# Optimization experiments

Hardware: AMD Instinct MI355X
Metric: run time of the kernel (lower is better)

The kernel has to match this reference:

```python
import jax, jax.numpy as jnp
import numpy as np

T, H, I, E, K = 4096, 2048, 1408, 8, 2


def setup_inputs() -> dict:
    key = jax.random.key(0)
    k1, k2, k3, k4, k5, k6 = jax.random.split(key, 6)
    hidden_states = jax.random.normal(k1, (T, H), dtype=jnp.float32)
    top_k_index = jax.random.randint(k2, (T, K), 0, E, dtype=jnp.int32)
    top_k_weights = jax.random.uniform(k3, (T, K), dtype=jnp.float32)
    # nn.Linear stores weight as [out_features, in_features]
    s_h = 1.0 / np.sqrt(H)
    s_i = 1.0 / np.sqrt(I)
    gate_w = jax.random.uniform(k4, (E, I, H), dtype=jnp.float32, minval=-s_h, maxval=s_h)
    up_w = jax.random.uniform(k5, (E, I, H), dtype=jnp.float32, minval=-s_h, maxval=s_h)
    down_w = jax.random.uniform(k6, (E, H, I), dtype=jnp.float32, minval=-s_i, maxval=s_i)
    return {
        "hidden_states": hidden_states,
        "top_k_index": top_k_index,
        "top_k_weights": top_k_weights,
        "gate_w": gate_w,
        "up_w": up_w,
        "down_w": down_w,
    }


def reference(hidden_states, top_k_index, top_k_weights, gate_w, up_w, down_w):
    # combine[t, e] = sum_k top_k_weights[t, k] * 1[top_k_index[t, k] == e]
    num_experts = gate_w.shape[0]
    one_hot = jax.nn.one_hot(top_k_index, num_experts, dtype=hidden_states.dtype)  # [T, K, E]
    combine = jnp.einsum("tk,tke->te", top_k_weights, one_hot)  # [T, E]

    # dense-equivalent of per-expert gather -> SwiGLU MLP -> scatter-add
    gate = jnp.einsum("th,eih->tei", hidden_states, gate_w)  # [T, E, I]
    up = jnp.einsum("th,eih->tei", hidden_states, up_w)      # [T, E, I]
    inter = jax.nn.silu(gate) * up                               # [T, E, I]
    out = jnp.einsum("te,tei,ehi->th", combine, inter, down_w)  # [T, H]
    return out
```

## Files before the change

kernel.cpp:

```cpp
#include <hip/hip_runtime.h>
#include <cstdint>
#include <cstddef>

#define T_TOK 4096
#define HD 2048
#define ID 1408
#define NE 8
#define NA (T_TOK * 2)
#define MAXR 9216
#define MAXT 80
#define EIH ((size_t)NE * ID * HD)
#define N4 ((int)(EIH / 4))
#define NCGU 2048
#define NCASTD 1024
#define NTILE_M (MAXR / 128)

typedef __bf16 bf16x8 __attribute__((ext_vector_type(8)));
typedef float f32x4 __attribute__((ext_vector_type(4)));

__device__ __forceinline__ unsigned short f2bf(float f) {
  union { float f; unsigned int u; } c; c.f = f;
  unsigned int u = c.u;
  u += 0x7fffu + ((u >> 16) & 1u);
  return (unsigned short)(u >> 16);
}

__device__ __forceinline__ void gl_lds16(const unsigned short* g, unsigned short* l) {
  __builtin_amdgcn_global_load_lds(
      (const __attribute__((address_space(1))) unsigned int*)g,
      (__attribute__((address_space(3))) unsigned int*)l, 16, 0, 0);
}

__device__ __forceinline__ int swz_off(int R, int fq) {
  int q = ((R & 1) << 2) | fq;
  int p = q ^ ((R >> 1) & 7);
  return (R >> 1) * 64 + p * 8;
}

__global__ void moe_count(const int* __restrict__ idx, int* __restrict__ cnt) {
  int a = blockIdx.x * 256 + threadIdx.x;
  if (a < NA) atomicAdd(&cnt[idx[a]], 1);
}

__global__ void moe_scan(const int* __restrict__ cnt, int* __restrict__ seg,
                         int* __restrict__ work_e, int* __restrict__ work_r,
                         int* __restrict__ ntiles) {
  if (blockIdx.x == 0 && threadIdx.x == 0) {
    int off = 0, nt = 0;
    for (int e = 0; e < NE; ++e) {
      seg[e] = off;
      int c = cnt[e];
      int tiles = (c + 127) >> 7;
      for (int tb = 0; tb < tiles; ++tb) {
        work_e[nt] = e;
        work_r[nt] = off + tb * 128;
        ++nt;
      }
      off += tiles << 7;
    }
    *ntiles = nt;
  }
}

__global__ void moe_fill(const int* __restrict__ idx, const float* __restrict__ wts,
                         const int* __restrict__ seg, int* __restrict__ cnt2,
                         int* __restrict__ row_token, float* __restrict__ row_weight,
                         int* __restrict__ slot_of) {
  int a = blockIdx.x * 256 + threadIdx.x;
  if (a < NA) {
    int e = idx[a];
    int pos = atomicAdd(&cnt2[e], 1);
    int slot = seg[e] + pos;
    row_token[slot] = a >> 1;
    row_weight[slot] = wts[a];
    slot_of[a] = slot;
  }
}

__global__ void mega_gather_castgu(
    const float* __restrict__ hidden, const int* __restrict__ slot_of,
    unsigned short* __restrict__ Xg,
    const float* __restrict__ gate_w, const float* __restrict__ up_w,
    unsigned short* __restrict__ gate_bf, unsigned short* __restrict__ ub_out) {
  const int bx = blockIdx.x;
  if (bx < NA) {
    const int slot = slot_of[bx];
    const int t = bx >> 1;
    const float4* src = (const float4*)(hidden + (size_t)t * HD);
    ushort4* dst = (ushort4*)(Xg + (size_t)slot * HD);
#pragma unroll
    for (int j = 0; j < 2; ++j) {
      int i = threadIdx.x + j * 256;
      float4 v = src[i];
      ushort4 o;
      o.x = f2bf(v.x); o.y = f2bf(v.y); o.z = f2bf(v.z); o.w = f2bf(v.w);
      dst[i] = o;
    }
  } else {
    const int cb = bx - NA;
    const int total = 2 * N4;
    for (int i = cb * 256 + threadIdx.x; i < total; i += NCGU * 256) {
      const float* s; unsigned short* t; int j = i;
      if (j < N4) { s = gate_w; t = gate_bf; }
      else { s = up_w; t = ub_out; j -= N4; }
      float4 v = ((const float4*)s)[j];
      ushort4 o;
      o.x = f2bf(v.x); o.y = f2bf(v.y); o.z = f2bf(v.z); o.w = f2bf(v.w);
      ((ushort4*)t)[j] = o;
    }
  }
}

__global__ __launch_bounds__(256, 2) void moe_gateup(
    const unsigned short* __restrict__ Xg,
    const unsigned short* __restrict__ Wg,
    const unsigned short* __restrict__ Wu,
    unsigned short* __restrict__ inter,
    const int* __restrict__ work_e, const int* __restrict__ work_r,
    const int* __restrict__ ntiles,
    const float* __restrict__ down_w, unsigned short* __restrict__ down_bf) {
  const int bx = blockIdx.x;
  if (bx < NCASTD) {
    for (int i = bx * 256 + threadIdx.x; i < N4; i += NCASTD * 256) {
      float4 v = ((const float4*)down_w)[i];
      ushort4 o;
      o.x = f2bf(v.x); o.y = f2bf(v.y); o.z = f2bf(v.z); o.w = f2bf(v.w);
      ((ushort4*)down_bf)[i] = o;
    }
    return;
  }
  const int t = bx - NCASTD;
  const int tile = t % NTILE_M;
  if (tile >= *ntiles) return;
  const int e = work_e[tile];
  const int row0 = work_r[tile];
  const int col0 = (t / NTILE_M) * 128;

  __shared__ unsigned short As[2][128 * 32];
  __shared__ unsigned short Bgs[2][128 * 32];
  __shared__ unsigned short Bus[2][128 * 32];

  const int tid = threadIdx.x;
  const int lane = tid & 63;
  const int wave = tid >> 6;
  const int wm = wave >> 1, wn = wave & 1;
  const int p_l = lane & 7;
  const int ub  = lane >> 3;
  const int q_l = p_l ^ ub;
  const int srow = (ub << 1) | (q_l >> 2);
  const int scol = (q_l & 3) << 3;
  const int fm = lane & 15, fq = lane >> 4;

  const size_t a_base = (size_t)row0 * HD;
  const size_t b_base = ((size_t)e * ID + col0) * HD;

  f32x4 zero = {0.f, 0.f, 0.f, 0.f};
  f32x4 accg[4][4], accu[4][4];
#pragma unroll
  for (int mi = 0; mi < 4; ++mi)
#pragma unroll
    for (int ni = 0; ni < 4; ++ni) { accg[mi][ni] = zero; accu[mi][ni] = zero; }

  for (int k0 = 0; k0 < HD; k0 += 64) {
#pragma unroll
    for (int s = 0; s < 2; ++s)
#pragma unroll
      for (int h = 0; h < 2; ++h) {
        const int m0 = wave * 32 + h * 16;
        const size_t go = (size_t)(m0 + srow) * HD + k0 + s * 32 + scol;
        gl_lds16(Xg + a_base + go, &As[s][m0 * 32]);
        gl_lds16(Wg + b_base + go, &Bgs[s][m0 * 32]);
        gl_lds16(Wu + b_base + go, &Bus[s][m0 * 32]);
      }
    __syncthreads();

#pragma unroll
    for (int ks = 0; ks < 2; ++ks) {
      bf16x8 a[4], bg[4], bu[4];
#pragma unroll
      for (int i = 0; i < 4; ++i) {
        a[i]  = *(const bf16x8*)&As[ks][swz_off(wm * 64 + i * 16 + fm, fq)];
        bg[i] = *(const bf16x8*)&Bgs[ks][swz_off(wn * 64 + i * 16 + fm, fq)];
        bu[i] = *(const bf16x8*)&Bus[ks][swz_off(wn * 64 + i * 16 + fm, fq)];
      }
#pragma unroll
      for (int mi = 0; mi < 4; ++mi)
#pragma unroll
        for (int ni = 0; ni < 4; ++ni) {
          accg[mi][ni] = __builtin_amdgcn_mfma_f32_16x16x32_bf16(a[mi], bg[ni], accg[mi][ni], 0, 0, 0);
          accu[mi][ni] = __builtin_amdgcn_mfma_f32_16x16x32_bf16(a[mi], bu[ni], accu[mi][ni], 0, 0, 0);
        }
    }
    __syncthreads();
  }

#pragma unroll
  for (int mi = 0; mi < 4; ++mi)
#pragma unroll
    for (int ni = 0; ni < 4; ++ni)
#pragma unroll
      for (int r = 0; r < 4; ++r) {
        float g = accg[mi][ni][r];
        float u = accu[mi][ni][r];
        float v = (g / (1.0f + __expf(-g))) * u;
        int row = row0 + wm * 64 + mi * 16 + fq * 4 + r;
        int col = col0 + wn * 64 + ni * 16 + fm;
        inter[(size_t)row * ID + col] = f2bf(v);
      }
}

__global__ __launch_bounds__(256, 2) void moe_down(
    const unsigned short* __restrict__ inter,
    const unsigned short* __restrict__ Wd,
    float* __restrict__ out,
    const int* __restrict__ work_e, const int* __restrict__ work_r,
    const int* __restrict__ ntiles,
    const int* __restrict__ row_token, const float* __restrict__ row_weight) {
  const int tile = blockIdx.x;
  if (tile >= *ntiles) return;
  const int e = work_e[tile];
  const int row0 = work_r[tile];
  const int col0 = blockIdx.y * 128;

  __shared__ unsigned short As[2][128 * 32];
  __shared__ unsigned short Bs[2][128 * 32];
  __shared__ int tok_s[128];
  __shared__ float w_s[128];

  const int tid = threadIdx.x;
  if (tid < 128) {
    tok_s[tid] = row_token[row0 + tid];
    w_s[tid] = row_weight[row0 + tid];
  }

  const int lane = tid & 63;
  const int wave = tid >> 6;
  const int wm = wave >> 1, wn = wave & 1;
  const int p_l = lane & 7;
  const int ub  = lane >> 3;
  const int q_l = p_l ^ ub;
  const int srow = (ub << 1) | (q_l >> 2);
  const int scol = (q_l & 3) << 3;
  const int fm = lane & 15, fq = lane >> 4;

  const size_t a_base = (size_t)row0 * ID;
  const size_t b_base = ((size_t)e * HD + col0) * ID;

  f32x4 zero = {0.f, 0.f, 0.f, 0.f};
  f32x4 acc[4][4];
#pragma unroll
  for (int mi = 0; mi < 4; ++mi)
#pragma unroll
    for (int ni = 0; ni < 4; ++ni) acc[mi][ni] = zero;

  for (int k0 = 0; k0 < ID; k0 += 64) {
#pragma unroll
    for (int s = 0; s < 2; ++s)
#pragma unroll
      for (int h = 0; h < 2; ++h) {
        const int m0 = wave * 32 + h * 16;
        const size_t go = (size_t)(m0 + srow) * ID + k0 + s * 32 + scol;
        gl_lds16(inter + a_base + go, &As[s][m0 * 32]);
        gl_lds16(Wd + b_base + go, &Bs[s][m0 * 32]);
      }
    __syncthreads();

#pragma unroll
    for (int ks = 0; ks < 2; ++ks) {
      bf16x8 a[4], b[4];
#pragma unroll
      for (int i = 0; i < 4; ++i) {
        a[i] = *(const bf16x8*)&As[ks][swz_off(wm * 64 + i * 16 + fm, fq)];
        b[i] = *(const bf16x8*)&Bs[ks][swz_off(wn * 64 + i * 16 + fm, fq)];
      }
#pragma unroll
      for (int mi = 0; mi < 4; ++mi)
#pragma unroll
        for (int ni = 0; ni < 4; ++ni)
          acc[mi][ni] = __builtin_amdgcn_mfma_f32_16x16x32_bf16(a[mi], b[ni], acc[mi][ni], 0, 0, 0);
    }
    __syncthreads();
  }

#pragma unroll
  for (int mi = 0; mi < 4; ++mi)
#pragma unroll
    for (int ni = 0; ni < 4; ++ni)
#pragma unroll
      for (int r = 0; r < 4; ++r) {
        int rl = wm * 64 + mi * 16 + fq * 4 + r;
        int tok = tok_s[rl];
        if (tok >= 0) {
          int col = col0 + wn * 64 + ni * 16 + fm;
          atomicAdd(&out[(size_t)tok * HD + col], w_s[rl] * acc[mi][ni][r]);
        }
      }
}

extern "C" void kernel_launch(void* const* d_in, const int* in_sizes, int n_in,
                              void* d_out, int out_size, void* d_ws, size_t ws_size,
                              hipStream_t stream) {
  const float* hidden = (const float*)d_in[0];
  const int* topk_idx = (const int*)d_in[1];
  const float* topk_w = (const float*)d_in[2];
  const float* gate_w = (const float*)d_in[3];
  const float* up_w = (const float*)d_in[4];
  const float* down_w = (const float*)d_in[5];
  float* out = (float*)d_out;

  char* ws = (char*)d_ws;
  size_t o_gate = 0;
  size_t o_up   = o_gate + EIH * 2;
  size_t o_down = o_up + EIH * 2;
  size_t o_xg   = o_down + EIH * 2;
  size_t o_int  = o_xg + (size_t)MAXR * HD * 2;
  size_t o_tok  = o_int + (size_t)MAXR * ID * 2;
  size_t o_wgt  = o_tok + (size_t)MAXR * 4;
  size_t o_slot = o_wgt + (size_t)MAXR * 4;
  size_t o_small = o_slot + (size_t)NA * 4;

  unsigned short* gate_bf = (unsigned short*)(ws + o_gate);
  unsigned short* up_bf   = (unsigned short*)(ws + o_up);
  unsigned short* down_bf = (unsigned short*)(ws + o_down);
  unsigned short* Xg      = (unsigned short*)(ws + o_xg);
  unsigned short* inter   = (unsigned short*)(ws + o_int);
  int* row_token = (int*)(ws + o_tok);
  float* row_weight = (float*)(ws + o_wgt);
  int* slot_of = (int*)(ws + o_slot);
  int* cnt    = (int*)(ws + o_small);
  int* cnt2   = cnt + 8;
  int* seg    = cnt + 16;
  int* ntiles = cnt + 24;
  int* work_e = cnt + 32;
  int* work_r = cnt + 32 + MAXT;

  hipMemsetAsync(out, 0, (size_t)T_TOK * HD * 4, stream);
  hipMemsetAsync(cnt, 0, (32 + 2 * MAXT) * 4, stream);
  hipMemsetAsync(row_token, 0xFF, (size_t)MAXR * 4, stream);

  moe_count<<<NA / 256, 256, 0, stream>>>(topk_idx, cnt);
  moe_scan<<<1, 64, 0, stream>>>(cnt, seg, work_e, work_r, ntiles);
  moe_fill<<<NA / 256, 256, 0, stream>>>(topk_idx, topk_w, seg, cnt2,
                                         row_token, row_weight, slot_of);

  mega_gather_castgu<<<NA + NCGU, 256, 0, stream>>>(hidden, slot_of, Xg,
                                                    gate_w, up_w, gate_bf, up_bf);

  moe_gateup<<<NCASTD + NTILE_M * (ID / 128), 256, 0, stream>>>(
      Xg, gate_bf, up_bf, inter, work_e, work_r, ntiles, down_w, down_bf);

  dim3 gridB(NTILE_M, HD / 128);
  moe_down<<<gridB, 256, 0, stream>>>(inter, down_bf, out, work_e, work_r, ntiles,
                                      row_token, row_weight);
}
```

Baseline: 664.7 us.

## Triple-buffer GEMM K-loop with async loads, reorder blocks, nontemporal cast loads

Both GEMM kernels move from a double-buffered 64-wide K step with two __syncthreads per step to a three-stage ring of 32-wide K slices. The next slice is issued before waiting with explicit vmcnt counts, so global-to-LDS loads overlap MFMA work, and s_setprio raises wave priority around the MFMA block. The gate/up kernel now places GEMM blocks before the down_w cast blocks and interleaves tile indices across groups of eight, and the fp32 cast loops use nontemporal loads. The hand-counted vmcnt values and the fixed iteration counts (62 and 42) are tied to the problem sizes, and the extra LDS stage may reduce occupancy.

```diff
diff --git a/kernel.cpp b/kernel.cpp
--- a/kernel.cpp
+++ b/kernel.cpp
@@ -14,6 +14,7 @@
 #define NCGU 2048
 #define NCASTD 1024
 #define NTILE_M (MAXR / 128)
+#define NGEMM_GU (NTILE_M * (ID / 128))
 
 typedef __bf16 bf16x8 __attribute__((ext_vector_type(8)));
 typedef float f32x4 __attribute__((ext_vector_type(4)));
@@ -103,9 +104,9 @@
       const float* s; unsigned short* t; int j = i;
       if (j < N4) { s = gate_w; t = gate_bf; }
       else { s = up_w; t = ub_out; j -= N4; }
-      float4 v = ((const float4*)s)[j];
+      f32x4 v = __builtin_nontemporal_load((const f32x4*)s + j);
       ushort4 o;
-      o.x = f2bf(v.x); o.y = f2bf(v.y); o.z = f2bf(v.z); o.w = f2bf(v.w);
+      o.x = f2bf(v[0]); o.y = f2bf(v[1]); o.z = f2bf(v[2]); o.w = f2bf(v[3]);
       ((ushort4*)t)[j] = o;
     }
   }
@@ -120,25 +121,26 @@
     const int* __restrict__ ntiles,
     const float* __restrict__ down_w, unsigned short* __restrict__ down_bf) {
   const int bx = blockIdx.x;
-  if (bx < NCASTD) {
-    for (int i = bx * 256 + threadIdx.x; i < N4; i += NCASTD * 256) {
-      float4 v = ((const float4*)down_w)[i];
+  if (bx >= NGEMM_GU) {
+    const int cb = bx - NGEMM_GU;
+    for (int i = cb * 256 + threadIdx.x; i < N4; i += NCASTD * 256) {
+      f32x4 v = __builtin_nontemporal_load((const f32x4*)down_w + i);
       ushort4 o;
-      o.x = f2bf(v.x); o.y = f2bf(v.y); o.z = f2bf(v.z); o.w = f2bf(v.w);
+      o.x = f2bf(v[0]); o.y = f2bf(v[1]); o.z = f2bf(v[2]); o.w = f2bf(v[3]);
       ((ushort4*)down_bf)[i] = o;
     }
     return;
   }
-  const int t = bx - NCASTD;
-  const int tile = t % NTILE_M;
+  const int g = (bx & 7) * (NGEMM_GU / 8) + (bx >> 3);
+  const int tile = g % NTILE_M;
   if (tile >= *ntiles) return;
   const int e = work_e[tile];
   const int row0 = work_r[tile];
-  const int col0 = (t / NTILE_M) * 128;
-
-  __shared__ unsigned short As[2][128 * 32];
-  __shared__ unsigned short Bgs[2][128 * 32];
-  __shared__ unsigned short Bus[2][128 * 32];
+  const int col0 = (g / NTILE_M) * 128;
+
+  __shared__ unsigned short As[3][128 * 32];
+  __shared__ unsigned short Bgs[3][128 * 32];
+  __shared__ unsigned short Bus[3][128 * 32];
 
   const int tid = threadIdx.x;
   const int lane = tid & 63;
@@ -161,38 +163,69 @@
 #pragma unroll
     for (int ni = 0; ni < 4; ++ni) { accg[mi][ni] = zero; accu[mi][ni] = zero; }
 
-  for (int k0 = 0; k0 < HD; k0 += 64) {
-#pragma unroll
-    for (int s = 0; s < 2; ++s)
-#pragma unroll
-      for (int h = 0; h < 2; ++h) {
-        const int m0 = wave * 32 + h * 16;
-        const size_t go = (size_t)(m0 + srow) * HD + k0 + s * 32 + scol;
-        gl_lds16(Xg + a_base + go, &As[s][m0 * 32]);
-        gl_lds16(Wg + b_base + go, &Bgs[s][m0 * 32]);
-        gl_lds16(Wu + b_base + go, &Bus[s][m0 * 32]);
+  int offA[4], offB[4];
+#pragma unroll
+  for (int i = 0; i < 4; ++i) {
+    offA[i] = swz_off(wm * 64 + i * 16 + fm, fq);
+    offB[i] = swz_off(wn * 64 + i * 16 + fm, fq);
+  }
+
+  auto stage = [&](int k0, int st) {
+#pragma unroll
+    for (int h = 0; h < 2; ++h) {
+      const int m0 = (wave << 5) + (h << 4);
+      const size_t go = (size_t)(m0 + srow) * HD + k0 + scol;
+      gl_lds16(Xg + a_base + go, &As[st][m0 * 32]);
+      gl_lds16(Wg + b_base + go, &Bgs[st][m0 * 32]);
+      gl_lds16(Wu + b_base + go, &Bus[st][m0 * 32]);
+    }
+  };
+
+  auto compute = [&](int st) {
+    bf16x8 a[4], bg[4], bu[4];
+#pragma unroll
+    for (int i = 0; i < 4; ++i) {
+      a[i]  = *(const bf16x8*)&As[st][offA[i]];
+      bg[i] = *(const bf16x8*)&Bgs[st][offB[i]];
+      bu[i] = *(const bf16x8*)&Bus[st][offB[i]];
+    }
+    __builtin_amdgcn_s_setprio(1);
+#pragma unroll
+    for (int mi = 0; mi < 4; ++mi)
+#pragma unroll
+      for (int ni = 0; ni < 4; ++ni) {
+        accg[mi][ni] = __builtin_amdgcn_mfma_f32_16x16x32_bf16(a[mi], bg[ni], accg[mi][ni], 0, 0, 0);
+        accu[mi][ni] = __builtin_amdgcn_mfma_f32_16x16x32_bf16(a[mi], bu[ni], accu[mi][ni], 0, 0, 0);
       }
-    __syncthreads();
-
-#pragma unroll
-    for (int ks = 0; ks < 2; ++ks) {
-      bf16x8 a[4], bg[4], bu[4];
-#pragma unroll
-      for (int i = 0; i < 4; ++i) {
-        a[i]  = *(const bf16x8*)&As[ks][swz_off(wm * 64 + i * 16 + fm, fq)];
-        bg[i] = *(const bf16x8*)&Bgs[ks][swz_off(wn * 64 + i * 16 + fm, fq)];
-        bu[i] = *(const bf16x8*)&Bus[ks][swz_off(wn * 64 + i * 16 + fm, fq)];
-      }
-#pragma unroll
-      for (int mi = 0; mi < 4; ++mi)
-#pragma unroll
-        for (int ni = 0; ni < 4; ++ni) {
-          accg[mi][ni] = __builtin_amdgcn_mfma_f32_16x16x32_bf16(a[mi], bg[ni], accg[mi][ni], 0, 0, 0);
-          accu[mi][ni] = __builtin_amdgcn_mfma_f32_16x16x32_bf16(a[mi], bu[ni], accu[mi][ni], 0, 0, 0);
-        }
-    }
-    __syncthreads();
-  }
+    __builtin_amdgcn_s_setprio(0);
+  };
+
+  stage(0, 0);
+  stage(32, 1);
+  int stc = 0, stp = 2, k0p = 64;
+#pragma unroll 1
+  for (int k = 0; k < 62; ++k) {
+    __builtin_amdgcn_s_barrier();
+    stage(k0p, stp);
+    asm volatile("s_waitcnt vmcnt(12)" ::: "memory");
+    __builtin_amdgcn_s_barrier();
+    __builtin_amdgcn_sched_barrier(0);
+    compute(stc);
+    __builtin_amdgcn_sched_barrier(0);
+    k0p += 32;
+    stc = (stc == 2) ? 0 : stc + 1;
+    stp = (stp == 2) ? 0 : stp + 1;
+  }
+  __builtin_amdgcn_s_barrier();
+  asm volatile("s_waitcnt vmcnt(6)" ::: "memory");
+  __builtin_amdgcn_s_barrier();
+  __builtin_amdgcn_sched_barrier(0);
+  compute(2);
+  __builtin_amdgcn_s_barrier();
+  asm volatile("s_waitcnt vmcnt(0)" ::: "memory");
+  __builtin_amdgcn_s_barrier();
+  __builtin_amdgcn_sched_barrier(0);
+  compute(0);
 
 #pragma unroll
   for (int mi = 0; mi < 4; ++mi)
@@ -200,9 +233,9 @@
     for (int ni = 0; ni < 4; ++ni)
 #pragma unroll
       for (int r = 0; r < 4; ++r) {
-        float g = accg[mi][ni][r];
+        float gg = accg[mi][ni][r];
         float u = accu[mi][ni][r];
-        float v = (g / (1.0f + __expf(-g))) * u;
+        float v = (gg / (1.0f + __expf(-gg))) * u;
         int row = row0 + wm * 64 + mi * 16 + fq * 4 + r;
         int col = col0 + wn * 64 + ni * 16 + fm;
         inter[(size_t)row * ID + col] = f2bf(v);
@@ -222,8 +255,8 @@
   const int row0 = work_r[tile];
   const int col0 = blockIdx.y * 128;
 
-  __shared__ unsigned short As[2][128 * 32];
-  __shared__ unsigned short Bs[2][128 * 32];
+  __shared__ unsigned short As[3][128 * 32];
+  __shared__ unsigned short Bs[3][128 * 32];
   __shared__ int tok_s[128];
   __shared__ float w_s[128];
 
@@ -253,34 +286,65 @@
 #pragma unroll
     for (int ni = 0; ni < 4; ++ni) acc[mi][ni] = zero;
 
-  for (int k0 = 0; k0 < ID; k0 += 64) {
-#pragma unroll
-    for (int s = 0; s < 2; ++s)
-#pragma unroll
-      for (int h = 0; h < 2; ++h) {
-        const int m0 = wave * 32 + h * 16;
-        const size_t go = (size_t)(m0 + srow) * ID + k0 + s * 32 + scol;
-        gl_lds16(inter + a_base + go, &As[s][m0 * 32]);
-        gl_lds16(Wd + b_base + go, &Bs[s][m0 * 32]);
-      }
-    __syncthreads();
-
-#pragma unroll
-    for (int ks = 0; ks < 2; ++ks) {
-      bf16x8 a[4], b[4];
-#pragma unroll
-      for (int i = 0; i < 4; ++i) {
-        a[i] = *(const bf16x8*)&As[ks][swz_off(wm * 64 + i * 16 + fm, fq)];
-        b[i] = *(const bf16x8*)&Bs[ks][swz_off(wn * 64 + i * 16 + fm, fq)];
-      }
-#pragma unroll
-      for (int mi = 0; mi < 4; ++mi)
-#pragma unroll
-        for (int ni = 0; ni < 4; ++ni)
-          acc[mi][ni] = __builtin_amdgcn_mfma_f32_16x16x32_bf16(a[mi], b[ni], acc[mi][ni], 0, 0, 0);
-    }
-    __syncthreads();
-  }
+  int offA[4], offB[4];
+#pragma unroll
+  for (int i = 0; i < 4; ++i) {
+    offA[i] = swz_off(wm * 64 + i * 16 + fm, fq);
+    offB[i] = swz_off(wn * 64 + i * 16 + fm, fq);
+  }
+
+  auto stage = [&](int k0, int st) {
+#pragma unroll
+    for (int h = 0; h < 2; ++h) {
+      const int m0 = (wave << 5) + (h << 4);
+      const size_t go = (size_t)(m0 + srow) * ID + k0 + scol;
+      gl_lds16(inter + a_base + go, &As[st][m0 * 32]);
+      gl_lds16(Wd + b_base + go, &Bs[st][m0 * 32]);
+    }
+  };
+
+  auto compute = [&](int st) {
+    bf16x8 a[4], b[4];
+#pragma unroll
+    for (int i = 0; i < 4; ++i) {
+      a[i] = *(const bf16x8*)&As[st][offA[i]];
+      b[i] = *(const bf16x8*)&Bs[st][offB[i]];
+    }
+    __builtin_amdgcn_s_setprio(1);
+#pragma unroll
+    for (int mi = 0; mi < 4; ++mi)
+#pragma unroll
+      for (int ni = 0; ni < 4; ++ni)
+        acc[mi][ni] = __builtin_amdgcn_mfma_f32_16x16x32_bf16(a[mi], b[ni], acc[mi][ni], 0, 0, 0);
+    __builtin_amdgcn_s_setprio(0);
+  };
+
+  stage(0, 0);
+  stage(32, 1);
+  int stc = 0, stp = 2, k0p = 64;
+#pragma unroll 1
+  for (int k = 0; k < 42; ++k) {
+    __builtin_amdgcn_s_barrier();
+    stage(k0p, stp);
+    asm volatile("s_waitcnt vmcnt(8)" ::: "memory");
+    __builtin_amdgcn_s_barrier();
+    __builtin_amdgcn_sched_barrier(0);
+    compute(stc);
+    __builtin_amdgcn_sched_barrier(0);
+    k0p += 32;
+    stc = (stc == 2) ? 0 : stc + 1;
+    stp = (stp == 2) ? 0 : stp + 1;
+  }
+  __builtin_amdgcn_s_barrier();
+  asm volatile("s_waitcnt vmcnt(4)" ::: "memory");
+  __builtin_amdgcn_s_barrier();
+  __builtin_amdgcn_sched_barrier(0);
+  compute(0);
+  __builtin_amdgcn_s_barrier();
+  asm volatile("s_waitcnt vmcnt(0)" ::: "memory");
+  __builtin_amdgcn_s_barrier();
+  __builtin_amdgcn_sched_barrier(0);
+  compute(1);
 
 #pragma unroll
   for (int mi = 0; mi < 4; ++mi)
@@ -346,7 +410,7 @@
   mega_gather_castgu<<<NA + NCGU, 256, 0, stream>>>(hidden, slot_of, Xg,
                                                     gate_w, up_w, gate_bf, up_bf);
 
-  moe_gateup<<<NCASTD + NTILE_M * (ID / 128), 256, 0, stream>>>(
+  moe_gateup<<<NGEMM_GU + NCASTD, 256, 0, stream>>>(
       Xg, gate_bf, up_bf, inter, work_e, work_r, ntiles, down_w, down_bf);
 
   dim3 gridB(NTILE_M, HD / 128);
```

Result: faster. 610.7 us (-8.1%).

## Enlarge MoE GEMM tiles to 256 rows with 8 waves and triple-buffered LDS pipeline

Applied to the files above, without the earlier changes.

Expert row segments are now padded to 256-row tiles. Both grouped GEMMs run with 512 threads (8 waves) and use a three-stage LDS ring with split A/B staging, explicit vmcnt waits, s_barrier and setprio around the MFMA blocks, so global loads overlap compute. The gate/up kernel puts the down-weight cast blocks after the GEMM blocks and remaps block ids for locality. Weight casts use nontemporal loads. The aim is more data reuse per tile and hidden load latency, at the cost of more padding waste, higher LDS use and fewer blocks in flight.

```diff
diff --git a/kernel.cpp b/kernel.cpp
--- a/kernel.cpp
+++ b/kernel.cpp
@@ -7,13 +7,16 @@
 #define ID 1408
 #define NE 8
 #define NA (T_TOK * 2)
-#define MAXR 9216
-#define MAXT 80
+#define MAXR 10240
+#define MAXT 40
 #define EIH ((size_t)NE * ID * HD)
 #define N4 ((int)(EIH / 4))
 #define NCGU 2048
-#define NCASTD 1024
-#define NTILE_M (MAXR / 128)
+#define NCASTD 512
+#define NTILE_G (MAXR / 256)
+#define NGEMM_GU (NTILE_G * (ID / 128))
+#define NKGU (HD / 32)
+#define NKD  (ID / 32)
 
 typedef __bf16 bf16x8 __attribute__((ext_vector_type(8)));
 typedef float f32x4 __attribute__((ext_vector_type(4)));
@@ -50,13 +53,13 @@
     for (int e = 0; e < NE; ++e) {
       seg[e] = off;
       int c = cnt[e];
-      int tiles = (c + 127) >> 7;
+      int tiles = (c + 255) >> 8;
       for (int tb = 0; tb < tiles; ++tb) {
         work_e[nt] = e;
-        work_r[nt] = off + tb * 128;
+        work_r[nt] = off + tb * 256;
         ++nt;
       }
-      off += tiles << 7;
+      off += tiles << 8;
     }
     *ntiles = nt;
   }
@@ -103,15 +106,15 @@
       const float* s; unsigned short* t; int j = i;
       if (j < N4) { s = gate_w; t = gate_bf; }
       else { s = up_w; t = ub_out; j -= N4; }
-      float4 v = ((const float4*)s)[j];
+      f32x4 v = __builtin_nontemporal_load((const f32x4*)s + j);
       ushort4 o;
-      o.x = f2bf(v.x); o.y = f2bf(v.y); o.z = f2bf(v.z); o.w = f2bf(v.w);
+      o.x = f2bf(v[0]); o.y = f2bf(v[1]); o.z = f2bf(v[2]); o.w = f2bf(v[3]);
       ((ushort4*)t)[j] = o;
     }
   }
 }
 
-__global__ __launch_bounds__(256, 2) void moe_gateup(
+__global__ __launch_bounds__(512, 2) void moe_gateup(
     const unsigned short* __restrict__ Xg,
     const unsigned short* __restrict__ Wg,
     const unsigned short* __restrict__ Wu,
@@ -120,30 +123,30 @@
     const int* __restrict__ ntiles,
     const float* __restrict__ down_w, unsigned short* __restrict__ down_bf) {
   const int bx = blockIdx.x;
-  if (bx < NCASTD) {
-    for (int i = bx * 256 + threadIdx.x; i < N4; i += NCASTD * 256) {
-      float4 v = ((const float4*)down_w)[i];
+  if (bx >= NGEMM_GU) {
+    const int cb = bx - NGEMM_GU;
+    for (int i = cb * 512 + threadIdx.x; i < N4; i += NCASTD * 512) {
+      f32x4 v = __builtin_nontemporal_load((const f32x4*)down_w + i);
       ushort4 o;
-      o.x = f2bf(v.x); o.y = f2bf(v.y); o.z = f2bf(v.z); o.w = f2bf(v.w);
+      o.x = f2bf(v[0]); o.y = f2bf(v[1]); o.z = f2bf(v[2]); o.w = f2bf(v[3]);
       ((ushort4*)down_bf)[i] = o;
     }
     return;
   }
-  const int t = bx - NCASTD;
-  const int tile = t % NTILE_M;
+  const int g = (bx & 7) * (NGEMM_GU / 8) + (bx >> 3);
+  const int tile = g % NTILE_G;
   if (tile >= *ntiles) return;
   const int e = work_e[tile];
   const int row0 = work_r[tile];
-  const int col0 = (t / NTILE_M) * 128;
-
-  __shared__ unsigned short As[2][128 * 32];
-  __shared__ unsigned short Bgs[2][128 * 32];
-  __shared__ unsigned short Bus[2][128 * 32];
+  const int col0 = (g / NTILE_G) * 128;
+
+  __shared__ unsigned short As[3][256 * 32];
+  __shared__ unsigned short Bs[3][256 * 32];
 
   const int tid = threadIdx.x;
   const int lane = tid & 63;
   const int wave = tid >> 6;
-  const int wm = wave >> 1, wn = wave & 1;
+  const int wm = wave >> 2, wn = wave & 3;
   const int p_l = lane & 7;
   const int ub  = lane >> 3;
   const int q_l = p_l ^ ub;
@@ -155,61 +158,101 @@
   const size_t b_base = ((size_t)e * ID + col0) * HD;
 
   f32x4 zero = {0.f, 0.f, 0.f, 0.f};
-  f32x4 accg[4][4], accu[4][4];
-#pragma unroll
-  for (int mi = 0; mi < 4; ++mi)
-#pragma unroll
-    for (int ni = 0; ni < 4; ++ni) { accg[mi][ni] = zero; accu[mi][ni] = zero; }
-
-  for (int k0 = 0; k0 < HD; k0 += 64) {
-#pragma unroll
-    for (int s = 0; s < 2; ++s)
-#pragma unroll
-      for (int h = 0; h < 2; ++h) {
-        const int m0 = wave * 32 + h * 16;
-        const size_t go = (size_t)(m0 + srow) * HD + k0 + s * 32 + scol;
-        gl_lds16(Xg + a_base + go, &As[s][m0 * 32]);
-        gl_lds16(Wg + b_base + go, &Bgs[s][m0 * 32]);
-        gl_lds16(Wu + b_base + go, &Bus[s][m0 * 32]);
+  f32x4 accg[8][2], accu[8][2];
+#pragma unroll
+  for (int mi = 0; mi < 8; ++mi)
+#pragma unroll
+    for (int ni = 0; ni < 2; ++ni) { accg[mi][ni] = zero; accu[mi][ni] = zero; }
+
+  auto stageA = [&](int k0, int b) {
+#pragma unroll
+    for (int j = 0; j < 2; ++j) {
+      const int rb = j * 128 + wave * 16;
+      gl_lds16(Xg + a_base + (size_t)(rb + srow) * HD + k0 + scol, &As[b][rb * 32]);
+    }
+  };
+  auto stageB = [&](int k0, int b) {
+    const int rb = wave * 16;
+    gl_lds16(Wg + b_base + (size_t)(rb + srow) * HD + k0 + scol, &Bs[b][rb * 32]);
+    gl_lds16(Wu + b_base + (size_t)(rb + srow) * HD + k0 + scol, &Bs[b][(128 + rb) * 32]);
+  };
+
+  stageA(0, 0); stageB(0, 0);
+  stageA(32, 1); stageB(32, 1);
+  asm volatile("s_waitcnt vmcnt(4)" ::: "memory");
+  __builtin_amdgcn_s_barrier();
+  __builtin_amdgcn_sched_barrier(0);
+
+  int bufc = 0, buf2 = 2, k2 = 64;
+  bf16x8 bg[2], bu[2];
+#pragma unroll 1
+  for (int t = 0; t < NKGU; ++t) {
+    if (t + 2 < NKGU) stageA(k2, buf2);
+    {
+      bf16x8 af[4];
+#pragma unroll
+      for (int i = 0; i < 2; ++i) {
+        bg[i] = *(const bf16x8*)&Bs[bufc][swz_off(wn * 32 + i * 16 + fm, fq)];
+        bu[i] = *(const bf16x8*)&Bs[bufc][swz_off(128 + wn * 32 + i * 16 + fm, fq)];
       }
-    __syncthreads();
-
-#pragma unroll
-    for (int ks = 0; ks < 2; ++ks) {
-      bf16x8 a[4], bg[4], bu[4];
-#pragma unroll
-      for (int i = 0; i < 4; ++i) {
-        a[i]  = *(const bf16x8*)&As[ks][swz_off(wm * 64 + i * 16 + fm, fq)];
-        bg[i] = *(const bf16x8*)&Bgs[ks][swz_off(wn * 64 + i * 16 + fm, fq)];
-        bu[i] = *(const bf16x8*)&Bus[ks][swz_off(wn * 64 + i * 16 + fm, fq)];
-      }
+#pragma unroll
+      for (int i = 0; i < 4; ++i)
+        af[i] = *(const bf16x8*)&As[bufc][swz_off(wm * 128 + i * 16 + fm, fq)];
+      __builtin_amdgcn_s_setprio(1);
 #pragma unroll
       for (int mi = 0; mi < 4; ++mi)
 #pragma unroll
-        for (int ni = 0; ni < 4; ++ni) {
-          accg[mi][ni] = __builtin_amdgcn_mfma_f32_16x16x32_bf16(a[mi], bg[ni], accg[mi][ni], 0, 0, 0);
-          accu[mi][ni] = __builtin_amdgcn_mfma_f32_16x16x32_bf16(a[mi], bu[ni], accu[mi][ni], 0, 0, 0);
+        for (int ni = 0; ni < 2; ++ni) {
+          accg[mi][ni] = __builtin_amdgcn_mfma_f32_16x16x32_bf16(af[mi], bg[ni], accg[mi][ni], 0, 0, 0);
+          accu[mi][ni] = __builtin_amdgcn_mfma_f32_16x16x32_bf16(af[mi], bu[ni], accu[mi][ni], 0, 0, 0);
         }
-    }
-    __syncthreads();
-  }
-
-#pragma unroll
-  for (int mi = 0; mi < 4; ++mi)
-#pragma unroll
-    for (int ni = 0; ni < 4; ++ni)
+      __builtin_amdgcn_s_setprio(0);
+    }
+    __builtin_amdgcn_s_barrier();
+    __builtin_amdgcn_sched_barrier(0);
+    if (t + 2 < NKGU) stageB(k2, buf2);
+    {
+      bf16x8 af[4];
+#pragma unroll
+      for (int i = 0; i < 4; ++i)
+        af[i] = *(const bf16x8*)&As[bufc][swz_off(wm * 128 + (4 + i) * 16 + fm, fq)];
+      __builtin_amdgcn_s_setprio(1);
+#pragma unroll
+      for (int mi = 0; mi < 4; ++mi)
+#pragma unroll
+        for (int ni = 0; ni < 2; ++ni) {
+          accg[4 + mi][ni] = __builtin_amdgcn_mfma_f32_16x16x32_bf16(af[mi], bg[ni], accg[4 + mi][ni], 0, 0, 0);
+          accu[4 + mi][ni] = __builtin_amdgcn_mfma_f32_16x16x32_bf16(af[mi], bu[ni], accu[4 + mi][ni], 0, 0, 0);
+        }
+      __builtin_amdgcn_s_setprio(0);
+    }
+    if (t < NKGU - 1) {
+      if (t + 2 < NKGU) asm volatile("s_waitcnt vmcnt(4)" ::: "memory");
+      else              asm volatile("s_waitcnt vmcnt(0)" ::: "memory");
+      __builtin_amdgcn_s_barrier();
+      __builtin_amdgcn_sched_barrier(0);
+    }
+    k2 += 32;
+    bufc = (bufc == 2) ? 0 : bufc + 1;
+    buf2 = (buf2 == 2) ? 0 : buf2 + 1;
+  }
+
+#pragma unroll
+  for (int mi = 0; mi < 8; ++mi)
+#pragma unroll
+    for (int ni = 0; ni < 2; ++ni)
 #pragma unroll
       for (int r = 0; r < 4; ++r) {
-        float g = accg[mi][ni][r];
+        float gg = accg[mi][ni][r];
         float u = accu[mi][ni][r];
-        float v = (g / (1.0f + __expf(-g))) * u;
-        int row = row0 + wm * 64 + mi * 16 + fq * 4 + r;
-        int col = col0 + wn * 64 + ni * 16 + fm;
+        float v = (gg / (1.0f + __expf(-gg))) * u;
+        int row = row0 + wm * 128 + mi * 16 + fq * 4 + r;
+        int col = col0 + wn * 32 + ni * 16 + fm;
         inter[(size_t)row * ID + col] = f2bf(v);
       }
 }
 
-__global__ __launch_bounds__(256, 2) void moe_down(
+__global__ __launch_bounds__(512, 2) void moe_down(
     const unsigned short* __restrict__ inter,
     const unsigned short* __restrict__ Wd,
     float* __restrict__ out,
@@ -220,22 +263,23 @@
   if (tile >= *ntiles) return;
   const int e = work_e[tile];
   const int row0 = work_r[tile];
-  const int col0 = blockIdx.y * 128;
-
-  __shared__ unsigned short As[2][128 * 32];
-  __shared__ unsigned short Bs[2][128 * 32];
-  __shared__ int tok_s[128];
-  __shared__ float w_s[128];
+  const int col0 = blockIdx.y * 256;
+
+  __shared__ unsigned short As[3][256 * 32];
+  __shared__ unsigned short Bs[3][256 * 32];
+  __shared__ int tok_s[256];
+  __shared__ float w_s[256];
 
   const int tid = threadIdx.x;
-  if (tid < 128) {
+  if (tid < 256) {
     tok_s[tid] = row_token[row0 + tid];
     w_s[tid] = row_weight[row0 + tid];
   }
+  __syncthreads();
 
   const int lane = tid & 63;
   const int wave = tid >> 6;
-  const int wm = wave >> 1, wn = wave & 1;
+  const int wm = wave >> 2, wn = wave & 3;
   const int p_l = lane & 7;
   const int ub  = lane >> 3;
   const int q_l = p_l ^ ub;
@@ -247,48 +291,88 @@
   const size_t b_base = ((size_t)e * HD + col0) * ID;
 
   f32x4 zero = {0.f, 0.f, 0.f, 0.f};
-  f32x4 acc[4][4];
-#pragma unroll
-  for (int mi = 0; mi < 4; ++mi)
+  f32x4 acc[8][4];
+#pragma unroll
+  for (int mi = 0; mi < 8; ++mi)
 #pragma unroll
     for (int ni = 0; ni < 4; ++ni) acc[mi][ni] = zero;
 
-  for (int k0 = 0; k0 < ID; k0 += 64) {
-#pragma unroll
-    for (int s = 0; s < 2; ++s)
-#pragma unroll
-      for (int h = 0; h < 2; ++h) {
-        const int m0 = wave * 32 + h * 16;
-        const size_t go = (size_t)(m0 + srow) * ID + k0 + s * 32 + scol;
-        gl_lds16(inter + a_base + go, &As[s][m0 * 32]);
-        gl_lds16(Wd + b_base + go, &Bs[s][m0 * 32]);
-      }
-    __syncthreads();
-
-#pragma unroll
-    for (int ks = 0; ks < 2; ++ks) {
-      bf16x8 a[4], b[4];
-#pragma unroll
-      for (int i = 0; i < 4; ++i) {
-        a[i] = *(const bf16x8*)&As[ks][swz_off(wm * 64 + i * 16 + fm, fq)];
-        b[i] = *(const bf16x8*)&Bs[ks][swz_off(wn * 64 + i * 16 + fm, fq)];
-      }
+  auto stageA = [&](int k0, int b) {
+#pragma unroll
+    for (int j = 0; j < 2; ++j) {
+      const int rb = j * 128 + wave * 16;
+      gl_lds16(inter + a_base + (size_t)(rb + srow) * ID + k0 + scol, &As[b][rb * 32]);
+    }
+  };
+  auto stageB = [&](int k0, int b) {
+#pragma unroll
+    for (int j = 0; j < 2; ++j) {
+      const int rb = j * 128 + wave * 16;
+      gl_lds16(Wd + b_base + (size_t)(rb + srow) * ID + k0 + scol, &Bs[b][rb * 32]);
+    }
+  };
+
+  stageA(0, 0); stageB(0, 0);
+  stageA(32, 1); stageB(32, 1);
+  asm volatile("s_waitcnt vmcnt(4)" ::: "memory");
+  __builtin_amdgcn_s_barrier();
+  __builtin_amdgcn_sched_barrier(0);
+
+  int bufc = 0, buf2 = 2, k2 = 64;
+  bf16x8 b4[4];
+#pragma unroll 1
+  for (int t = 0; t < NKD; ++t) {
+    if (t + 2 < NKD) stageA(k2, buf2);
+    {
+      bf16x8 af[4];
+#pragma unroll
+      for (int i = 0; i < 4; ++i)
+        b4[i] = *(const bf16x8*)&Bs[bufc][swz_off(wn * 64 + i * 16 + fm, fq)];
+#pragma unroll
+      for (int i = 0; i < 4; ++i)
+        af[i] = *(const bf16x8*)&As[bufc][swz_off(wm * 128 + i * 16 + fm, fq)];
+      __builtin_amdgcn_s_setprio(1);
 #pragma unroll
       for (int mi = 0; mi < 4; ++mi)
 #pragma unroll
         for (int ni = 0; ni < 4; ++ni)
-          acc[mi][ni] = __builtin_amdgcn_mfma_f32_16x16x32_bf16(a[mi], b[ni], acc[mi][ni], 0, 0, 0);
-    }
-    __syncthreads();
-  }
-
-#pragma unroll
-  for (int mi = 0; mi < 4; ++mi)
+          acc[mi][ni] = __builtin_amdgcn_mfma_f32_16x16x32_bf16(af[mi], b4[ni], acc[mi][ni], 0, 0, 0);
+      __builtin_amdgcn_s_setprio(0);
+    }
+    __builtin_amdgcn_s_barrier();
+    __builtin_amdgcn_sched_barrier(0);
+    if (t + 2 < NKD) stageB(k2, buf2);
+    {
+      bf16x8 af[4];
+#pragma unroll
+      for (int i = 0; i < 4; ++i)
+        af[i] = *(const bf16x8*)&As[bufc][swz_off(wm * 128 + (4 + i) * 16 + fm, fq)];
+      __builtin_amdgcn_s_setprio(1);
+#pragma unroll
+      for (int mi = 0; mi < 4; ++mi)
+#pragma unroll
+        for (int ni = 0; ni < 4; ++ni)
+          acc[4 + mi][ni] = __builtin_amdgcn_mfma_f32_16x16x32_bf16(af[mi], b4[ni], acc[4 + mi][ni], 0, 0, 0);
+      __builtin_amdgcn_s_setprio(0);
+    }
+    if (t < NKD - 1) {
+      if (t + 2 < NKD) asm volatile("s_waitcnt vmcnt(4)" ::: "memory");
+      else             asm volatile("s_waitcnt vmcnt(0)" ::: "memory");
+      __builtin_amdgcn_s_barrier();
+      __builtin_amdgcn_sched_barrier(0);
+    }
+    k2 += 32;
+    bufc = (bufc == 2) ? 0 : bufc + 1;
+    buf2 = (buf2 == 2) ? 0 : buf2 + 1;
+  }
+
+#pragma unroll
+  for (int mi = 0; mi < 8; ++mi)
 #pragma unroll
     for (int ni = 0; ni < 4; ++ni)
 #pragma unroll
       for (int r = 0; r < 4; ++r) {
-        int rl = wm * 64 + mi * 16 + fq * 4 + r;
+        int rl = wm * 128 + mi * 16 + fq * 4 + r;
         int tok = tok_s[rl];
         if (tok >= 0) {
           int col = col0 + wn * 64 + ni * 16 + fm;
@@ -346,10 +430,10 @@
   mega_gather_castgu<<<NA + NCGU, 256, 0, stream>>>(hidden, slot_of, Xg,
                                                     gate_w, up_w, gate_bf, up_bf);
 
-  moe_gateup<<<NCASTD + NTILE_M * (ID / 128), 256, 0, stream>>>(
+  moe_gateup<<<NGEMM_GU + NCASTD, 512, 0, stream>>>(
       Xg, gate_bf, up_bf, inter, work_e, work_r, ntiles, down_w, down_bf);
 
-  dim3 gridB(NTILE_M, HD / 128);
-  moe_down<<<gridB, 256, 0, stream>>>(inter, down_bf, out, work_e, work_r, ntiles,
+  dim3 gridB(NTILE_G, HD / 256);
+  moe_down<<<gridB, 512, 0, stream>>>(inter, down_bf, out, work_e, work_r, ntiles,
                                       row_token, row_weight);
 }
```

After: 652.1 us. No clear change (-1.9%).
